# Performance work log

Hardware: AMD Instinct MI355X
Metric: run time of the kernel (lower is better)

The kernel has to match this reference:

```python
import math
import jax, jax.numpy as jnp
import numpy as np
from jax import lax

RAY_START, RAY_END = 0.5, 2.5
N_PLANES = 32

# ---- camera constants (faithful to pose_spherical / fibonacci_sphere / ImagePlanes init) ----

def _pose_spherical_np(theta, phi, radius):
    trans_t = np.array([[1,0,0,0],[0,1,0,0],[0,0,1,radius],[0,0,0,1]], dtype=np.float64)
    p = phi/180.0*np.pi
    rot_phi = np.array([[1,0,0,0],[0,np.cos(p),-np.sin(p),0],[0,np.sin(p),np.cos(p),0],[0,0,0,1]], dtype=np.float64)
    t = theta/180.0*np.pi
    rot_theta = np.array([[np.cos(t),0,-np.sin(t),0],[0,1,0,0],[np.sin(t),0,np.cos(t),0],[0,0,0,1]], dtype=np.float64)
    e = 90.0/180.0*np.pi
    rot_eta = np.array([[np.cos(e),np.sin(e),0,0],[-np.sin(e),np.cos(e),0,0],[0,0,1,0],[0,0,0,1]], dtype=np.float64)
    c2w = rot_eta @ (rot_theta @ (rot_phi @ trans_t))
    return np.array([[-1,0,0,0],[0,0,1,0],[0,1,0,0],[0,0,0,1]], dtype=np.float64) @ c2w

def _fibonacci_sphere(n):
    pts = []
    golden = math.pi*(math.sqrt(5.0)-1.0)
    for i in range(n):
        y = 1 - (i/float(n-1))*2
        r = math.sqrt(1-y*y)
        th = golden*i
        x, z = math.cos(th)*r, math.sin(th)*r
        pts.append((math.atan2(z, math.sqrt(x*x+y*y)), math.atan2(y, x)))
    return pts

_poses = np.stack([_pose_spherical_np(theta, phi, -1.307) for phi, theta in _fibonacci_sphere(N_PLANES)])
_flip = np.diag(np.array([-1.0,1.0,1.0,1.0]))
POSES34 = jnp.asarray(np.stack([np.linalg.inv(p @ _flip)[:3] for p in _poses]).astype(np.float32))  # [32,3,4]
KMAT = jnp.asarray(np.array([[1.0254,0,0.5],[0,1.0254,0.5],[0,0,1]], dtype=np.float32))  # [3,3]

# ---- grid_sample(bilinear, zeros, align_corners=False) ----

def _grid_sample(img, grid):
    # img [C,H,W], grid [P,2] (x,y) in [-1,1] -> [C,P]
    C, H, W = img.shape
    ix = ((grid[:, 0] + 1.0)*W - 1.0)*0.5
    iy = ((grid[:, 1] + 1.0)*H - 1.0)*0.5
    x0 = jnp.floor(ix); y0 = jnp.floor(iy)
    wx1 = ix - x0; wy1 = iy - y0
    def tap(xx, yy, w):
        valid = (xx >= 0) & (xx <= W - 1) & (yy >= 0) & (yy <= H - 1)
        xi = jnp.clip(xx, 0, W - 1).astype(jnp.int32)
        yi = jnp.clip(yy, 0, H - 1).astype(jnp.int32)
        return img[:, yi, xi] * (w*valid)[None, :]
    return (tap(x0, y0, (1-wx1)*(1-wy1)) + tap(x0+1, y0, wx1*(1-wy1))
            + tap(x0, y0+1, (1-wx1)*wy1) + tap(x0+1, y0+1, wx1*wy1))

# ---- ImagePlanes.forward ----

def _image_plane_feats(images, points):
    # images [32,3,H,W], points [P,3] -> [P, 96+64]
    P = points.shape[0]
    ph = jnp.concatenate([points, jnp.ones((P, 1), points.dtype)], axis=1)  # [P,4]
    cam = jnp.einsum('kij,pj->kip', POSES34, ph)            # [32,3,P]
    ps = jnp.einsum('ij,kjp->kip', KMAT, cam)                # [32,3,P]
    pix = jnp.clip(ps[:, :2, :] / ps[:, 2:3, :], 0.0, 1.0)*2.0 - 1.0  # [32,2,P]
    grid = jnp.transpose(pix, (0, 2, 1))                     # [32,P,2]
    feats = jax.vmap(_grid_sample)(images, grid)             # [32,3,P]
    feats = jnp.transpose(feats, (2, 0, 1)).reshape(P, -1)   # [P,96] plane-major
    pixflat = jnp.transpose(grid, (1, 0, 2)).reshape(P, -1)  # [P,64]
    return jnp.concatenate([feats, pixflat], axis=1)

# ---- RenderNetwork.forward (only self.net path is used) ----

def _decode(x, W1, b1, W2, b2):
    h = jax.nn.softplus(x @ W1 + b1)
    o = h @ W2 + b2
    rgb = jax.nn.sigmoid(o[..., 1:])*(1.0 + 2*0.001) - 0.001
    return rgb, o[..., 0:1]

# ---- MipRayMarcher2 ----

def _ray_march(colors, densities, depths):
    deltas = depths[:, :, 1:] - depths[:, :, :-1]
    cm = (colors[:, :, :-1] + colors[:, :, 1:])*0.5
    dm = (densities[:, :, :-1] + densities[:, :, 1:])*0.5
    zm = (depths[:, :, :-1] + depths[:, :, 1:])*0.5
    dm = jax.nn.softplus(dm - 1.0)
    alpha = 1.0 - jnp.exp(-dm*deltas)
    shifted = jnp.concatenate([jnp.ones_like(alpha[:, :, :1]), 1.0 - alpha + 1e-10], axis=2)
    weights = alpha * jnp.cumprod(shifted, axis=2)[:, :, :-1]
    rgb = jnp.sum(weights*cm, axis=2)*2.0 - 1.0
    wtot = jnp.sum(weights, axis=2)
    depth = jnp.sum(weights*zm, axis=2)/wtot
    depth = jnp.clip(jnp.where(jnp.isnan(depth), jnp.inf, depth), jnp.min(depths), jnp.max(depths))
    return rgb, depth, weights

# ---- importance sampling (sample_pdf + maxpool/avgpool smoothing) ----

def _sample_pdf(bins, weights, u, eps=1e-5):
    M = weights.shape[-1]
    weights = weights + eps
    pdf = weights / jnp.sum(weights, -1, keepdims=True)
    cdf = jnp.cumsum(pdf, -1)
    cdf = jnp.concatenate([jnp.zeros_like(cdf[:, :1]), cdf], -1)  # [R,M+1]
    inds = jax.vmap(lambda c, uu: jnp.searchsorted(c, uu, side='right'))(cdf, u)
    below = jnp.maximum(inds - 1, 0)
    above = jnp.minimum(inds, M)
    cdf_b = jnp.take_along_axis(cdf, below, 1)
    cdf_a = jnp.take_along_axis(cdf, above, 1)
    bins_b = jnp.take_along_axis(bins, below, 1)
    bins_a = jnp.take_along_axis(bins, above, 1)
    denom = jnp.where(cdf_a - cdf_b < eps, 1.0, cdf_a - cdf_b)
    return bins_b + (u - cdf_b)/denom*(bins_a - bins_b)

def _sample_importance(z_vals, weights, n_imp, u):
    B, N, S, _ = z_vals.shape
    z = z_vals.reshape(B*N, S)
    w = weights.reshape(B*N, S - 1)
    wp = jnp.pad(w, ((0, 0), (1, 1)), constant_values=-jnp.inf)
    m = jnp.maximum(wp[:, :-1], wp[:, 1:])          # max_pool1d(k=2,s=1,p=1)
    sm = (m[:, :-1] + m[:, 1:])*0.5 + 0.01           # avg_pool1d(k=2,s=1)
    samples = _sample_pdf(z, sm[:, 1:-1], u.reshape(B*N, n_imp))
    return lax.stop_gradient(samples).reshape(B, N, n_imp, 1)

# ---- full ImportanceRenderer.forward ----

def _forward(planes, ray_origins, ray_directions, strat_noise, pdf_u, W1, b1, W2, b2, D, n_imp):
    B, N = ray_origins.shape[0], ray_origins.shape[1]
    H, Wd = planes.shape[-2], planes.shape[-1]
    images = planes.reshape(B, N_PLANES, 3, H, Wd)
    delta = (RAY_END - RAY_START)/(D - 1)
    depths_c = jnp.linspace(RAY_START, RAY_END, D, dtype=planes.dtype).reshape(1, 1, D, 1) + strat_noise*delta

    def run_pass(depths):
        S = depths.shape[2]
        pts = (ray_origins[:, :, None, :] + depths*ray_directions[:, :, None, :]).reshape(B, N*S, 3)
        feats = jax.vmap(_image_plane_feats)(images, pts)  # [B,N*S,160]
        rgb, sigma = _decode(feats, W1, b1, W2, b2)
        return rgb.reshape(B, N, S, 32), sigma.reshape(B, N, S, 1)

    colors_c, dens_c = run_pass(depths_c)
    _, _, w_c = _ray_march(colors_c, dens_c, depths_c)
    depths_f = _sample_importance(depths_c, w_c, n_imp, pdf_u)
    colors_f, dens_f = run_pass(depths_f)

    all_d = jnp.concatenate([depths_c, depths_f], axis=2)
    all_c = jnp.concatenate([colors_c, colors_f], axis=2)
    all_s = jnp.concatenate([dens_c, dens_f], axis=2)
    order = jnp.argsort(all_d[..., 0], axis=2)[..., None]
    all_d = jnp.take_along_axis(all_d, order, axis=2)
    all_c = jnp.take_along_axis(all_c, order, axis=2)
    all_s = jnp.take_along_axis(all_s, order, axis=2)
    rgb_final, depth_final, w = _ray_march(all_c, all_s, all_d)
    return jnp.concatenate([rgb_final, depth_final, jnp.sum(w, axis=2)], axis=-1)  # [B,N,34]


def setup_inputs() -> dict:
    key = jax.random.key(0)
    ks = jax.random.split(key, 7)
    B, N, D, NI, H = 2, 4096, 48, 48, 64
    rd = jax.random.normal(ks[2], (B, N, 3), jnp.float32)
    rd = rd / jnp.linalg.norm(rd, axis=-1, keepdims=True)
    return {
        'planes': jax.random.normal(ks[0], (B, 96, H, H), jnp.float32),
        'ray_origins': jax.random.normal(ks[1], (B, N, 3), jnp.float32)*0.1,
        'ray_directions': rd,
        'strat_noise': jax.random.uniform(ks[3], (B, N, D, 1), jnp.float32),
        'pdf_u': jax.random.uniform(ks[4], (B, N, NI), jnp.float32),
        'W1': jax.random.normal(ks[5], (160, 64), jnp.float32)*0.05,
        'b1': jnp.zeros((64,), jnp.float32),
        'W2': jax.random.normal(ks[6], (64, 33), jnp.float32)*0.05,
        'b2': jnp.zeros((33,), jnp.float32),
        'depth_resolution': 48,
        'N_importance': 48,
    }


def reference(planes, ray_origins, ray_directions, strat_noise, pdf_u, W1, b1, W2, b2, depth_resolution, N_importance):
    return _forward(planes, ray_origins, ray_directions, strat_noise, pdf_u, W1, b1, W2, b2, depth_resolution, N_importance)
```

## Files before the change

kernel.cpp:

```cpp
#include <hip/hip_runtime.h>
#include <math.h>

#define B_   2
#define N_   4096
#define S_   48
#define NPL  32
#define NRAYS (B_*N_)
#define NPTS  (NRAYS*S_)
#define DELTA_ (2.0f/47.0f)
#define NBLK_FUSED (NPTS/256)

#define ST_XS    65
#define ST_YS    66
#define ST_PLANE (ST_YS*ST_XS)
#define SETUP_GRID 66

#define OFF_POSES  0
#define OFF_MINMAX 384
#define OFF_W1E    512
#define OFF_W2E    8704
#define OFF_B2E    10240
#define OFF_ST     16384
#define OFF_PTS    1114624
#define OFF_DC     2687488
#define OFF_DF     3080704
#define OFF_SC     3473920
#define OFF_SF     3867136
#define OFF_CC     4260352
#define OFF_CF     10551808

typedef __attribute__((ext_vector_type(8))) short short8;
typedef __attribute__((ext_vector_type(4))) float f32x4;
typedef __attribute__((ext_vector_type(2))) float f32x2;

__device__ __forceinline__ float softplus_f(float x) {
    return fmaxf(x, 0.f) + __logf(1.f + __expf(-fabsf(x)));
}
__device__ __forceinline__ float sigmoid_f(float x) {
    return __builtin_amdgcn_rcpf(1.f + __expf(-x));
}
__device__ __forceinline__ unsigned short bf16rne(float x) {
    unsigned u = __float_as_uint(x);
    u += 0x7FFFu + ((u >> 16) & 1u);
    return (unsigned short)(u >> 16);
}
__device__ __forceinline__ unsigned bf16pk(float lo, float hi) {
    return (unsigned)bf16rne(lo) | ((unsigned)bf16rne(hi) << 16);
}
__device__ __forceinline__ float bf2f(unsigned short v) {
    return __uint_as_float(((unsigned)v) << 16);
}
__device__ __forceinline__ float bflo(unsigned u) { return __uint_as_float(u << 16); }
__device__ __forceinline__ float bfhi(unsigned u) { return __uint_as_float(u & 0xffff0000u); }
__device__ __forceinline__ f32x2 unpk2(unsigned u) { return (f32x2){bflo(u), bfhi(u)}; }

__global__ __launch_bounds__(256) void k_setup(
    float* ws, const float* __restrict__ W1,
    const float* __restrict__ W2, const float* __restrict__ b2,
    const float* __restrict__ planes, const float* __restrict__ noise)
{
    __shared__ unsigned short texs[3][4096];
    __shared__ float smn[4], smx[4];
    int bid = blockIdx.x;
    int t = threadIdx.x;
    if (bid == 0) {
        unsigned short* w1e = (unsigned short*)(ws + OFF_W1E);
        for (int o = t; o < 64*256; o += 256) {
            int chunk = o >> 9, lane = (o >> 3) & 63, j = o & 7;
            int s = chunk >> 2, nt = chunk & 3, q = lane >> 4, n = lane & 15;
            int nn = nt*16 + n;
            int p = s*4 + q;
            float v = 0.f;
            if (j < 3)      v = W1[(3*p+j)*64 + nn];
            else if (j < 5) v = W1[(96 + 2*p + (j-3))*64 + nn];
            w1e[o] = bf16rne(v);
        }
        unsigned short* w2e = (unsigned short*)(ws + OFF_W2E);
        for (int o = t; o < 6*512; o += 256) {
            int chunk = o >> 9, lane = (o >> 3) & 63, j = o & 7;
            int nt = chunk >> 1, s2 = chunk & 1, q = lane >> 4, n = lane & 15;
            int nn = nt*16 + n;
            int k2 = s2*32 + q*8 + j;
            float v = (nn < 33) ? W2[k2*33 + nn] : 0.f;
            w2e[o] = bf16rne(v);
        }
        for (int idx = t; idx < 48; idx += 256)
            ws[OFF_B2E + idx] = (idx < 33) ? b2[idx] : 0.f;
    } else if (bid == 1) {
        float mn = 1e30f, mx = -1e30f;
        for (int r = t; r < NRAYS; r += 256) {
            float n0  = noise[(size_t)r*48];
            float n47 = noise[(size_t)r*48 + 47];
            mn = fminf(mn, 0.5f + n0*DELTA_);
            mx = fmaxf(mx, 0.5f + 47.f*DELTA_ + n47*DELTA_);
        }
        for (int off = 32; off > 0; off >>= 1) {
            mn = fminf(mn, __shfl_down(mn, off));
            mx = fmaxf(mx, __shfl_down(mx, off));
        }
        if ((t & 63) == 0) { smn[t >> 6] = mn; smx[t >> 6] = mx; }
        __syncthreads();
        if (t == 0) {
            ws[OFF_MINMAX]     = fminf(fminf(smn[0], smn[1]), fminf(smn[2], smn[3]));
            ws[OFF_MINMAX + 1] = fmaxf(fmaxf(smx[0], smx[1]), fmaxf(smx[2], smx[3]));
        }
    } else {
        int bp = bid - 2;
        int b = bp >> 5, p = bp & 31;
        const float* base = planes + ((size_t)b*96 + 3*p)*4096;
        for (int i = t; i < 4096; i += 256) {
            texs[0][i] = bf16rne(base[i]);
            texs[1][i] = bf16rne(base[4096 + i]);
            texs[2][i] = bf16rne(base[8192 + i]);
        }
        __syncthreads();
        uint4* qd = (uint4*)(ws + OFF_ST) + (size_t)bp*ST_PLANE;
        for (int e = t; e < ST_PLANE; e += 256) {
            int y = e / ST_XS, x = e - y*ST_XS;
            int jy = y - 1;
            unsigned a01 = 0, a2 = 0, b01 = 0, b2v = 0;
            if (jy >= 0 && jy <= 63) {
                int jxa = x - 1, jxb = x;
                if (jxa >= 0 && jxa <= 63) {
                    int ti = jy*64 + jxa;
                    a01 = (unsigned)texs[0][ti] | ((unsigned)texs[1][ti] << 16);
                    a2  = (unsigned)texs[2][ti];
                }
                if (jxb <= 63) {
                    int ti = jy*64 + jxb;
                    b01 = (unsigned)texs[0][ti] | ((unsigned)texs[1][ti] << 16);
                    b2v = (unsigned)texs[2][ti];
                }
            }
            qd[e] = make_uint4(a01, a2, b01, b2v);
        }
    }
}

__device__ __forceinline__ void proj_pt(
    const f32x2 Px, const f32x2 Py, const f32x2 Pz, const f32x2 Pw, const f32x4 Pc,
    float px, float py, float pz,
    int& eoff, float& wx, float& wy, unsigned& gpk)
{
    f32x2 c01 = Pz*pz + Pw;
    c01 = Py*py + c01;
    c01 = Px*px + c01;
    float c2 = fmaf(Pc.x,px, fmaf(Pc.y,py, fmaf(Pc.z,pz, Pc.w)));
    float rz = __builtin_amdgcn_rcpf(c2);
    f32x2 t01 = c01*1.0254f + 0.5f*c2;
    t01 = t01*rz;
    float cx = fminf(fmaxf(t01.x, 0.f), 1.f);
    float cy = fminf(fmaxf(t01.y, 0.f), 1.f);
    float gx = fmaf(2.f, cx, -1.f);
    float gy = fmaf(2.f, cy, -1.f);
    float ixp = fmaf(64.f, cx, 0.5f);
    float iyp = fmaf(64.f, cy, 0.5f);
    float xf = floorf(ixp), yf = floorf(iyp);
    wx = ixp - xf; wy = iyp - yf;
    eoff = (int)yf*ST_XS + (int)xf;
    gpk = bf16pk(gx, gy);
}

__device__ __forceinline__ void bilerp_pack(
    const uint4 r0, const uint4 r1, float wx, float wy, unsigned gpk, uint4& av)
{
    float wy0 = 1.f - wy, wy1 = wy;
    float w0x = 1.f - wx, w1x = wx;
    f32x2 tl01 = unpk2(r0.x)*wy0 + unpk2(r1.x)*wy1;
    float tl2  = fmaf(wy0, bflo(r0.y), wy1*bflo(r1.y));
    f32x2 tr01 = unpk2(r0.z)*wy0 + unpk2(r1.z)*wy1;
    float tr2  = fmaf(wy0, bflo(r0.w), wy1*bflo(r1.w));
    f32x2 f01 = tl01*w0x + tr01*w1x;
    float f2  = fmaf(w0x, tl2, w1x*tr2);
    av.x = bf16pk(f01.x, f01.y);
    av.y = ((unsigned)bf16rne(f2)) | (gpk << 16);
    av.z = gpk >> 16;
    av.w = 0u;
}

__global__ __launch_bounds__(512, 4) void k_fused(
    const uint4* __restrict__ stq, const float4* __restrict__ pts,
    const float* __restrict__ poses,
    const float* __restrict__ b1, const unsigned short* __restrict__ w1e,
    const unsigned short* __restrict__ w2e, const float* __restrict__ b2e,
    unsigned short* __restrict__ colors, float* __restrict__ dens,
    const float* __restrict__ noise, const float* __restrict__ ro,
    const float* __restrict__ rd, float* __restrict__ dcout, int coarse)
{
    __shared__ __align__(16) unsigned short w1s[16384];
    __shared__ __align__(16) unsigned short w2s[3072];
    __shared__ __align__(16) unsigned short smem[8][1152];
    __shared__ __align__(16) float pl[384];
    int tid = threadIdx.x;
    int wv = tid >> 6, lane = tid & 63;
    int n = lane & 15, q = lane >> 4;
    int bid = blockIdx.x;
    int swz = (bid & 7)*(NBLK_FUSED/8) + (bid >> 3);
    int wlocal = swz*256 + wv*32;
    int bq = (wlocal >= NPTS/2) ? 32 : 0;

    {
        const uint4* g1 = (const uint4*)w1e;
        uint4* d1 = (uint4*)w1s;
        for (int i = tid; i < 2048; i += 512) d1[i] = g1[i];
        const uint4* g2 = (const uint4*)w2e;
        uint4* d2 = (uint4*)w2s;
        if (tid < 384) { d2[tid] = g2[tid]; pl[tid] = poses[tid]; }
    }
    __syncthreads();

    float px[2], py[2], pz[2];
    if (coarse) {
#pragma unroll
        for (int t = 0; t < 2; t++) {
            int pt = wlocal + t*16 + n;
            int ray = (int)(((unsigned)(pt >> 4) * 43691u) >> 17);
            int j = pt - ray*48;
            float depth = 0.5f + (float)j*DELTA_ + noise[pt]*DELTA_;
            px[t] = fmaf(depth, rd[ray*3+0], ro[ray*3+0]);
            py[t] = fmaf(depth, rd[ray*3+1], ro[ray*3+1]);
            pz[t] = fmaf(depth, rd[ray*3+2], ro[ray*3+2]);
            if (q == 0) dcout[pt] = depth;
        }
    } else {
#pragma unroll
        for (int t = 0; t < 2; t++) {
            float4 pv = pts[wlocal + t*16 + n];
            px[t] = pv.x; py[t] = pv.y; pz[t] = pv.z;
        }
    }

    f32x4 acc[2][4];
#pragma unroll
    for (int t = 0; t < 2; t++)
#pragma unroll
        for (int nt = 0; nt < 4; nt++) {
            float bv = b1[nt*16 + n];
            acc[t][nt] = (f32x4){bv, bv, bv, bv};
        }

#pragma unroll
    for (int s = 0; s < 8; s++) {
        int plane = s*4 + q;
        const float* Pp = pl + plane*12;
        f32x2 Px = *(const f32x2*)(Pp);
        f32x2 Py = *(const f32x2*)(Pp + 2);
        f32x2 Pz = *(const f32x2*)(Pp + 4);
        f32x2 Pw = *(const f32x2*)(Pp + 6);
        f32x4 Pc = *(const f32x4*)(Pp + 8);
        const uint4* stp = stq + (unsigned)(bq + plane)*(unsigned)ST_PLANE;
        union { short8 s8; uint4 u; } av[2];
        {
            int eo0, eo1; float wx0, wy0, wx1, wy1; unsigned g0, g1;
            proj_pt(Px, Py, Pz, Pw, Pc, px[0], py[0], pz[0], eo0, wx0, wy0, g0);
            proj_pt(Px, Py, Pz, Pw, Pc, px[1], py[1], pz[1], eo1, wx1, wy1, g1);
            uint4 a0 = stp[eo0], a1 = stp[eo0 + ST_XS];
            uint4 b0 = stp[eo1], b1r = stp[eo1 + ST_XS];
            bilerp_pack(a0, a1, wx0, wy0, g0, av[0].u);
            bilerp_pack(b0, b1r, wx1, wy1, g1, av[1].u);
        }
#pragma unroll
        for (int nt = 0; nt < 4; nt++) {
            short8 bfw = *(const short8*)(w1s + ((s*4 + nt) << 9) + (lane << 3));
#pragma unroll
            for (int t = 0; t < 2; t++)
                acc[t][nt] = __builtin_amdgcn_mfma_f32_16x16x32_bf16(av[t].s8, bfw, acc[t][nt], 0, 0, 0);
        }
    }

    short8 b2f[3][2];
#pragma unroll
    for (int nt = 0; nt < 3; nt++)
#pragma unroll
        for (int s2 = 0; s2 < 2; s2++)
            b2f[nt][s2] = *(const short8*)(w2s + (((nt << 1) | s2) << 9) + (lane << 3));

    unsigned short* ht = &smem[wv][0];
#pragma unroll
    for (int t = 0; t < 2; t++) {
#pragma unroll
        for (int nt = 0; nt < 4; nt++)
#pragma unroll
            for (int r = 0; r < 4; r++) {
                float hv = softplus_f(acc[t][nt][r]);
                ht[(q*4 + r)*72 + nt*16 + n] = bf16rne(hv);
            }
        short8 a2[2];
#pragma unroll
        for (int s2 = 0; s2 < 2; s2++)
            a2[s2] = *(const short8*)(ht + n*72 + s2*32 + q*8);

        f32x4 acc2[3];
#pragma unroll
        for (int nt = 0; nt < 3; nt++) {
            float bv = b2e[nt*16 + n];
            acc2[nt] = (f32x4){bv, bv, bv, bv};
        }
#pragma unroll
        for (int nt = 0; nt < 3; nt++)
#pragma unroll
            for (int s2 = 0; s2 < 2; s2++)
                acc2[nt] = __builtin_amdgcn_mfma_f32_16x16x32_bf16(a2[s2], b2f[nt][s2], acc2[nt], 0, 0, 0);

        float* ot = (float*)ht;
#pragma unroll
        for (int nt = 0; nt < 3; nt++) {
            int col = nt*16 + n;
#pragma unroll
            for (int r = 0; r < 4; r++) {
                float v = acc2[nt][r];
                int row = q*4 + r;
                if (col == 0) ot[row*34 + 32] = v;
                else if (col <= 32) {
                    float sg = sigmoid_f(v);
                    ot[row*34 + (col-1)] = fmaf(sg, 1.002f, -0.001f);
                }
            }
        }
        unsigned* cgu = (unsigned*)(colors + (size_t)(wlocal + t*16)*32);
#pragma unroll
        for (int i = 0; i < 4; i++) {
            int ui = i*64 + lane;
            int pt = ui >> 4, ch = (ui & 15)*2;
            cgu[ui] = bf16pk(ot[pt*34 + ch], ot[pt*34 + ch + 1]);
        }
        if (lane < 16) dens[wlocal + t*16 + lane] = ot[lane*34 + 32];
    }
}

__global__ __launch_bounds__(256) void k_imp(const float* __restrict__ u, float* ws,
                                             const float* __restrict__ ro,
                                             const float* __restrict__ rd,
                                             float4* __restrict__ pts) {
    __shared__ float zl[4][48];
    __shared__ float cdfl[4][46];
    int tid = threadIdx.x;
    int wv = tid >> 6, lane = tid & 63;
    int r = blockIdx.x*4 + wv;
    const float* z   = ws + OFF_DC + (size_t)r*48;
    const float* den = ws + OFF_SC + (size_t)r*48;
    float zv = 0.f, dv = 0.f;
    if (lane < 48) { zv = z[lane]; dv = den[lane]; zl[wv][lane] = zv; }
    float zn  = __shfl_down(zv, 1);
    float dnn = __shfl_down(dv, 1);
    float alpha = 0.f, f = 1.f;
    if (lane < 47) {
        float sp = softplus_f(0.5f*(dv + dnn) - 1.f);
        alpha = 1.f - __expf(-sp*(zn - zv));
        f = 1.f - alpha + 1e-10f;
    }
    float v = f;
    for (int off = 1; off < 64; off <<= 1) { float o = __shfl_up(v, off); if (lane >= off) v *= o; }
    float T = __shfl_up(v, 1); if (lane == 0) T = 1.f;
    float w = alpha*T;
    float wn1 = __shfl_down(w, 1), wn2 = __shfl_down(w, 2);
    float pw = 0.f;
    if (lane < 45) pw = 0.5f*(fmaxf(w, wn1) + fmaxf(wn1, wn2)) + 0.01f + 1e-5f;
    float s = pw;
    for (int off = 1; off < 64; off <<= 1) { float o = __shfl_up(s, off); if (lane >= off) s += o; }
    float csum = __shfl(s, 63);
    if (lane < 45) cdfl[wv][lane+1] = s/csum;
    if (lane == 63) cdfl[wv][0] = 0.f;
    __syncthreads();
    if (lane < 48) {
        float uu = u[(size_t)r*48 + lane];
        int lo = 0, hi = 46;
        while (lo < hi) { int mid = (lo+hi)>>1; if (uu >= cdfl[wv][mid]) lo = mid+1; else hi = mid; }
        int below = max(lo-1, 0), above = min(lo, 45);
        float cb = cdfl[wv][below], ca = cdfl[wv][above];
        float zb = zl[wv][below],   za = zl[wv][above];
        float dn2 = ca - cb; if (dn2 < 1e-5f) dn2 = 1.f;
        float df_s = zb + (uu - cb)/dn2*(za - zb);
        ws[OFF_DF + (size_t)r*48 + lane] = df_s;
        float fx = fmaf(df_s, rd[r*3+0], ro[r*3+0]);
        float fy = fmaf(df_s, rd[r*3+1], ro[r*3+1]);
        float fz = fmaf(df_s, rd[r*3+2], ro[r*3+2]);
        pts[(size_t)r*48 + lane] = make_float4(fx, fy, fz, df_s);
    }
}

__global__ __launch_bounds__(256) void k_final(float* __restrict__ out, const float* __restrict__ ws,
                                               const unsigned short* __restrict__ cC,
                                               const unsigned short* __restrict__ cF)
{
    __shared__ float kd[4][96];
    __shared__ float kden[4][96];
    __shared__ float sdl[4][96];
    __shared__ float sdenl[4][96];
    __shared__ int   sidxl[4][96];
    __shared__ float warr[4][96];
    __shared__ float earr[4][96];
    int tid = threadIdx.x;
    int wv = tid >> 6, lane = tid & 63;
    int r = blockIdx.x*4 + wv;
    const float* dc = ws + OFF_DC + (size_t)r*48;
    const float* df = ws + OFF_DF + (size_t)r*48;
    const float* sc = ws + OFF_SC + (size_t)r*48;
    const float* sf = ws + OFF_SF + (size_t)r*48;
    for (int i = lane; i < 96; i += 64) {
        float d, dn;
        if (i < 48) { d = dc[i]; dn = sc[i]; }
        else        { d = df[i-48]; dn = sf[i-48]; }
        kd[wv][i] = d; kden[wv][i] = dn;
    }
    __syncthreads();
    for (int i = lane; i < 96; i += 64) {
        float d = kd[wv][i];
        int rank = 0;
        for (int j = 0; j < 96; j++) {
            float dj = kd[wv][j];
            rank += (int)((dj < d) | ((dj == d) & (j < i)));
        }
        sdl[wv][rank] = d; sdenl[wv][rank] = kden[wv][i]; sidxl[wv][rank] = i;
    }
    __syncthreads();
    int i2 = 2*lane;
    float a0=0.f, f0=1.f, a1=0.f, f1=1.f, d0=0.f, d1=0.f, d2=0.f;
    if (i2 < 95) {
        d0 = sdl[wv][i2]; d1 = sdl[wv][i2+1];
        float sp = softplus_f(0.5f*(sdenl[wv][i2] + sdenl[wv][i2+1]) - 1.f);
        a0 = 1.f - __expf(-sp*(d1 - d0)); f0 = 1.f - a0 + 1e-10f;
    }
    if (i2+1 < 95) {
        d2 = sdl[wv][i2+2];
        float sp = softplus_f(0.5f*(sdenl[wv][i2+1] + sdenl[wv][i2+2]) - 1.f);
        a1 = 1.f - __expf(-sp*(d2 - d1)); f1 = 1.f - a1 + 1e-10f;
    }
    float p = f0*f1, v = p;
    for (int off = 1; off < 64; off <<= 1) { float o = __shfl_up(v, off); if (lane >= off) v *= o; }
    float excl = __shfl_up(v, 1); if (lane == 0) excl = 1.f;
    float w0 = a0*excl, w1 = a1*excl*f0;
    if (i2   < 96) warr[wv][i2]   = w0;
    if (i2+1 < 96) warr[wv][i2+1] = w1;
    float wsm = w0 + w1;
    float dsm = w0*0.5f*(d0+d1) + w1*0.5f*(d1+d2);
    for (int off = 32; off; off >>= 1) { wsm += __shfl_xor(wsm, off); dsm += __shfl_xor(dsm, off); }
    __syncthreads();
    for (int i = lane; i < 96; i += 64) {
        float wp = (i > 0)  ? warr[wv][i-1] : 0.f;
        float wc = (i < 95) ? warr[wv][i]   : 0.f;
        earr[wv][sidxl[wv][i]] = 0.5f*(wp + wc);
    }
    __syncthreads();
    int ch = lane & 31, half = lane >> 5;
    const unsigned short* cbase = (half ? cF : cC) + ((size_t)r*48)*32 + ch;
    const float* eb = &earr[wv][half*48];
    float a = 0.f;
    for (int jj = 0; jj < 48; jj++)
        a = fmaf(eb[jj], bf2f(cbase[(size_t)jj*32]), a);
    a += __shfl_xor(a, 32);
    if (lane < 32) out[(size_t)r*34 + lane] = 2.f*a - 1.f;
    if (lane == 0) {
        float gmn = ws[OFF_MINMAX];
        float gmx = ws[OFF_MINMAX + 1];
        float depth = dsm/wsm;
        if (depth != depth) depth = __builtin_inff();
        depth = fminf(fmaxf(depth, gmn), gmx);
        out[(size_t)r*34 + 32] = depth;
        out[(size_t)r*34 + 33] = wsm;
    }
}

static void h_mul3(const double* a, const double* b, double* o) {
    for (int i = 0; i < 3; i++)
        for (int j = 0; j < 3; j++) {
            double s = 0.0;
            for (int k = 0; k < 3; k++) s += a[i*3+k]*b[k*3+j];
            o[i*3+j] = s;
        }
}

static float h_poses[384];
static bool h_poses_init = false;

static void compute_poses_host() {
    for (int t = 0; t < 32; t++) {
        double y = 1.0 - (t/31.0)*2.0;
        double rr = sqrt(fmax(1.0 - y*y, 0.0));
        double golden = M_PI*(sqrt(5.0) - 1.0);
        double th = golden*(double)t;
        double x = cos(th)*rr, z = sin(th)*rr;
        double phi   = atan2(z, sqrt(x*x + y*y));
        double theta = atan2(y, x);
        double p  = phi/180.0*M_PI;
        double tt = theta/180.0*M_PI;
        double e  = 90.0/180.0*M_PI;
        double cp = cos(p), sp = sin(p), ct = cos(tt), st = sin(tt);
        double ce = cos(e), se = sin(e);
        double Ph[9] = {1,0,0,  0,cp,-sp,  0,sp,cp};
        double Th[9] = {ct,0,-st,  0,1,0,  st,0,ct};
        double Et[9] = {ce,se,0,  -se,ce,0,  0,0,1};
        double M3[9] = {-1,0,0,  0,0,1,  0,1,0};
        double A[9], Bm[9], R[9];
        h_mul3(Th, Ph, A);
        h_mul3(Et, A, Bm);
        h_mul3(M3, Bm, R);
        double radius = -1.307;
        double tv0 = radius*R[2], tv1 = radius*R[5], tv2 = radius*R[8];
        double Rf[9] = {-R[0],R[1],R[2], -R[3],R[4],R[5], -R[6],R[7],R[8]};
        float rowv[3][4];
        for (int j = 0; j < 3; j++) {
            double r0 = Rf[0*3+j], r1 = Rf[1*3+j], r2 = Rf[2*3+j];
            rowv[j][0] = (float)r0;
            rowv[j][1] = (float)r1;
            rowv[j][2] = (float)r2;
            rowv[j][3] = (float)(-(r0*tv0 + r1*tv1 + r2*tv2));
        }
        float* P = h_poses + t*12;
        P[0] = rowv[0][0]; P[1] = rowv[1][0];
        P[2] = rowv[0][1]; P[3] = rowv[1][1];
        P[4] = rowv[0][2]; P[5] = rowv[1][2];
        P[6] = rowv[0][3]; P[7] = rowv[1][3];
        P[8] = rowv[2][0]; P[9] = rowv[2][1]; P[10] = rowv[2][2]; P[11] = rowv[2][3];
    }
}

extern "C" void kernel_launch(void* const* d_in, const int* in_sizes, int n_in,
                              void* d_out, int out_size, void* d_ws, size_t ws_size,
                              hipStream_t stream) {
    const float* planes = (const float*)d_in[0];
    const float* ro     = (const float*)d_in[1];
    const float* rd     = (const float*)d_in[2];
    const float* noise  = (const float*)d_in[3];
    const float* u      = (const float*)d_in[4];
    const float* W1     = (const float*)d_in[5];
    const float* b1     = (const float*)d_in[6];
    const float* W2     = (const float*)d_in[7];
    const float* b2     = (const float*)d_in[8];
    float* ws  = (float*)d_ws;
    float* out = (float*)d_out;
    const unsigned short* w1e = (const unsigned short*)(ws + OFF_W1E);
    const unsigned short* w2e = (const unsigned short*)(ws + OFF_W2E);
    const uint4* stq = (const uint4*)(ws + OFF_ST);
    float4* pts = (float4*)(ws + OFF_PTS);
    unsigned short* cC = (unsigned short*)(ws + OFF_CC);
    unsigned short* cF = (unsigned short*)(ws + OFF_CF);

    if (!h_poses_init) { compute_poses_host(); h_poses_init = true; }
    hipMemcpyAsync(ws + OFF_POSES, h_poses, sizeof(h_poses),
                   hipMemcpyHostToDevice, stream);

    hipLaunchKernelGGL(k_setup, dim3(SETUP_GRID), dim3(256), 0, stream,
                       ws, W1, W2, b2, planes, noise);
    hipLaunchKernelGGL(k_fused, dim3(NBLK_FUSED), dim3(512), 0, stream,
                       stq, pts, ws + OFF_POSES, b1, w1e, w2e, ws + OFF_B2E, cC, ws + OFF_SC,
                       noise, ro, rd, ws + OFF_DC, 1);
    hipLaunchKernelGGL(k_imp, dim3(NRAYS/4), dim3(256), 0, stream, u, ws, ro, rd, pts);
    hipLaunchKernelGGL(k_fused, dim3(NBLK_FUSED), dim3(512), 0, stream,
                       stq, pts, ws + OFF_POSES, b1, w1e, w2e, ws + OFF_B2E, cF, ws + OFF_SF,
                       noise, ro, rd, ws + OFF_DC, 0);
    hipLaunchKernelGGL(k_final, dim3(NRAYS/4), dim3(256), 0, stream, out, ws, cC, cF);
}
```

Baseline: 227.4 us.

## Fuse importance sampling into fine pass and compute camera poses on device

After: 224.1 us. About the same (-1.4%).

```diff
diff --git a/kernel.cpp b/kernel.cpp
--- a/kernel.cpp
+++ b/kernel.cpp
@@ -21,13 +21,12 @@
 #define OFF_W2E    8704
 #define OFF_B2E    10240
 #define OFF_ST     16384
-#define OFF_PTS    1114624
-#define OFF_DC     2687488
-#define OFF_DF     3080704
-#define OFF_SC     3473920
-#define OFF_SF     3867136
-#define OFF_CC     4260352
-#define OFF_CF     10551808
+#define OFF_DC     1114624
+#define OFF_DF     1507840
+#define OFF_SC     1901056
+#define OFF_SF     2294272
+#define OFF_CC     2687488
+#define OFF_CF     8978944
 
 typedef __attribute__((ext_vector_type(8))) short short8;
 typedef __attribute__((ext_vector_type(4))) float f32x4;
@@ -53,6 +52,18 @@
 __device__ __forceinline__ float bflo(unsigned u) { return __uint_as_float(u << 16); }
 __device__ __forceinline__ float bfhi(unsigned u) { return __uint_as_float(u & 0xffff0000u); }
 __device__ __forceinline__ f32x2 unpk2(unsigned u) { return (f32x2){bflo(u), bfhi(u)}; }
+__device__ __forceinline__ int div48(int pt) {
+    return (int)(((unsigned)(pt >> 4) * 43691u) >> 17);
+}
+
+__device__ void mul3(const double* a, const double* b, double* o) {
+    for (int i = 0; i < 3; i++)
+        for (int j = 0; j < 3; j++) {
+            double s = 0.0;
+            for (int k = 0; k < 3; k++) s += a[i*3+k]*b[k*3+j];
+            o[i*3+j] = s;
+        }
+}
 
 __global__ __launch_bounds__(256) void k_setup(
     float* ws, const float* __restrict__ W1,
@@ -64,6 +75,45 @@
     int bid = blockIdx.x;
     int t = threadIdx.x;
     if (bid == 0) {
+        if (t < 32) {
+            double y = 1.0 - (t/31.0)*2.0;
+            double rr = sqrt(fmax(1.0 - y*y, 0.0));
+            double golden = M_PI*(sqrt(5.0) - 1.0);
+            double th = golden*(double)t;
+            double x = cos(th)*rr, z = sin(th)*rr;
+            double phi   = atan2(z, sqrt(x*x + y*y));
+            double theta = atan2(y, x);
+            double p  = phi/180.0*M_PI;
+            double tt = theta/180.0*M_PI;
+            double e  = 90.0/180.0*M_PI;
+            double cp = cos(p), sp = sin(p), ct = cos(tt), st = sin(tt);
+            double ce = cos(e), se = sin(e);
+            double Ph[9] = {1,0,0,  0,cp,-sp,  0,sp,cp};
+            double Th[9] = {ct,0,-st,  0,1,0,  st,0,ct};
+            double Et[9] = {ce,se,0,  -se,ce,0,  0,0,1};
+            double M3[9] = {-1,0,0,  0,0,1,  0,1,0};
+            double A[9], Bm[9], R[9];
+            mul3(Th, Ph, A);
+            mul3(Et, A, Bm);
+            mul3(M3, Bm, R);
+            double radius = -1.307;
+            double tv0 = radius*R[2], tv1 = radius*R[5], tv2 = radius*R[8];
+            double Rf[9] = {-R[0],R[1],R[2], -R[3],R[4],R[5], -R[6],R[7],R[8]};
+            float rowv[3][4];
+            for (int j = 0; j < 3; j++) {
+                double r0 = Rf[0*3+j], r1 = Rf[1*3+j], r2 = Rf[2*3+j];
+                rowv[j][0] = (float)r0;
+                rowv[j][1] = (float)r1;
+                rowv[j][2] = (float)r2;
+                rowv[j][3] = (float)(-(r0*tv0 + r1*tv1 + r2*tv2));
+            }
+            float* P = ws + OFF_POSES + t*12;
+            P[0] = rowv[0][0]; P[1] = rowv[1][0];
+            P[2] = rowv[0][1]; P[3] = rowv[1][1];
+            P[4] = rowv[0][2]; P[5] = rowv[1][2];
+            P[6] = rowv[0][3]; P[7] = rowv[1][3];
+            P[8] = rowv[2][0]; P[9] = rowv[2][1]; P[10] = rowv[2][2]; P[11] = rowv[2][3];
+        }
         unsigned short* w1e = (unsigned short*)(ws + OFF_W1E);
         for (int o = t; o < 64*256; o += 256) {
             int chunk = o >> 9, lane = (o >> 3) & 63, j = o & 7;
@@ -179,25 +229,29 @@
 }
 
 __global__ __launch_bounds__(512, 4) void k_fused(
-    const uint4* __restrict__ stq, const float4* __restrict__ pts,
-    const float* __restrict__ poses,
+    const uint4* __restrict__ stq, const float* __restrict__ poses,
     const float* __restrict__ b1, const unsigned short* __restrict__ w1e,
     const unsigned short* __restrict__ w2e, const float* __restrict__ b2e,
     unsigned short* __restrict__ colors, float* __restrict__ dens,
     const float* __restrict__ noise, const float* __restrict__ ro,
-    const float* __restrict__ rd, float* __restrict__ dcout, int coarse)
+    const float* __restrict__ rd, const float* __restrict__ u,
+    float* __restrict__ ws, int coarse)
 {
     __shared__ __align__(16) unsigned short w1s[16384];
     __shared__ __align__(16) unsigned short w2s[3072];
     __shared__ __align__(16) unsigned short smem[8][1152];
     __shared__ __align__(16) float pl[384];
+    __shared__ float impz[6][48];
+    __shared__ float impcdf[6][46];
+    __shared__ __align__(16) float4 posl[6][48];
     int tid = threadIdx.x;
     int wv = tid >> 6, lane = tid & 63;
     int n = lane & 15, q = lane >> 4;
     int bid = blockIdx.x;
     int swz = (bid & 7)*(NBLK_FUSED/8) + (bid >> 3);
     int wlocal = swz*256 + wv*32;
-    int bq = (wlocal >= NPTS/2) ? 32 : 0;
+    int bq = (swz*256 >= NPTS/2) ? 32 : 0;
+    int r0 = (int)(((unsigned)(swz*16) * 43691u) >> 17);
 
     {
         const uint4* g1 = (const uint4*)w1e;
@@ -207,6 +261,49 @@
         uint4* d2 = (uint4*)w2s;
         if (tid < 384) { d2[tid] = g2[tid]; pl[tid] = poses[tid]; }
     }
+
+    if (!coarse && wv < 6) {
+        int r = r0 + wv;
+        const float* z   = ws + OFF_DC + (size_t)r*48;
+        const float* den = ws + OFF_SC + (size_t)r*48;
+        float zv = 0.f, dv = 0.f;
+        if (lane < 48) { zv = z[lane]; dv = den[lane]; impz[wv][lane] = zv; }
+        float zn  = __shfl_down(zv, 1);
+        float dnn = __shfl_down(dv, 1);
+        float alpha = 0.f, f = 1.f;
+        if (lane < 47) {
+            float sp = softplus_f(0.5f*(dv + dnn) - 1.f);
+            alpha = 1.f - __expf(-sp*(zn - zv));
+            f = 1.f - alpha + 1e-10f;
+        }
+        float v = f;
+        for (int off = 1; off < 64; off <<= 1) { float o = __shfl_up(v, off); if (lane >= off) v *= o; }
+        float T = __shfl_up(v, 1); if (lane == 0) T = 1.f;
+        float w = alpha*T;
+        float wn1 = __shfl_down(w, 1), wn2 = __shfl_down(w, 2);
+        float pw = 0.f;
+        if (lane < 45) pw = 0.5f*(fmaxf(w, wn1) + fmaxf(wn1, wn2)) + 0.01f + 1e-5f;
+        float s = pw;
+        for (int off = 1; off < 64; off <<= 1) { float o = __shfl_up(s, off); if (lane >= off) s += o; }
+        float csum = __shfl(s, 63);
+        if (lane < 45) impcdf[wv][lane+1] = s/csum;
+        if (lane == 63) impcdf[wv][0] = 0.f;
+        if (lane < 48) {
+            float uu = u[(size_t)r*48 + lane];
+            int lo = 0, hi = 46;
+            while (lo < hi) { int mid = (lo+hi)>>1; if (uu >= impcdf[wv][mid]) lo = mid+1; else hi = mid; }
+            int below = max(lo-1, 0), above = min(lo, 45);
+            float cb = impcdf[wv][below], ca = impcdf[wv][above];
+            float zb = impz[wv][below],   za = impz[wv][above];
+            float dn2 = ca - cb; if (dn2 < 1e-5f) dn2 = 1.f;
+            float df_s = zb + (uu - cb)/dn2*(za - zb);
+            ws[OFF_DF + (size_t)r*48 + lane] = df_s;
+            float fx = fmaf(df_s, rd[r*3+0], ro[r*3+0]);
+            float fy = fmaf(df_s, rd[r*3+1], ro[r*3+1]);
+            float fz = fmaf(df_s, rd[r*3+2], ro[r*3+2]);
+            posl[wv][lane] = make_float4(fx, fy, fz, df_s);
+        }
+    }
     __syncthreads();
 
     float px[2], py[2], pz[2];
@@ -214,18 +311,20 @@
 #pragma unroll
         for (int t = 0; t < 2; t++) {
             int pt = wlocal + t*16 + n;
-            int ray = (int)(((unsigned)(pt >> 4) * 43691u) >> 17);
+            int ray = div48(pt);
             int j = pt - ray*48;
             float depth = 0.5f + (float)j*DELTA_ + noise[pt]*DELTA_;
             px[t] = fmaf(depth, rd[ray*3+0], ro[ray*3+0]);
             py[t] = fmaf(depth, rd[ray*3+1], ro[ray*3+1]);
             pz[t] = fmaf(depth, rd[ray*3+2], ro[ray*3+2]);
-            if (q == 0) dcout[pt] = depth;
+            if (q == 0) ws[OFF_DC + pt] = depth;
         }
     } else {
 #pragma unroll
         for (int t = 0; t < 2; t++) {
-            float4 pv = pts[wlocal + t*16 + n];
+            int pt = wlocal + t*16 + n;
+            int ray = div48(pt);
+            float4 pv = posl[ray - r0][pt - ray*48];
             px[t] = pv.x; py[t] = pv.y; pz[t] = pv.z;
         }
     }
@@ -325,57 +424,6 @@
             cgu[ui] = bf16pk(ot[pt*34 + ch], ot[pt*34 + ch + 1]);
         }
         if (lane < 16) dens[wlocal + t*16 + lane] = ot[lane*34 + 32];
-    }
-}
-
-__global__ __launch_bounds__(256) void k_imp(const float* __restrict__ u, float* ws,
-                                             const float* __restrict__ ro,
-                                             const float* __restrict__ rd,
-                                             float4* __restrict__ pts) {
-    __shared__ float zl[4][48];
-    __shared__ float cdfl[4][46];
-    int tid = threadIdx.x;
-    int wv = tid >> 6, lane = tid & 63;
-    int r = blockIdx.x*4 + wv;
-    const float* z   = ws + OFF_DC + (size_t)r*48;
-    const float* den = ws + OFF_SC + (size_t)r*48;
-    float zv = 0.f, dv = 0.f;
-    if (lane < 48) { zv = z[lane]; dv = den[lane]; zl[wv][lane] = zv; }
-    float zn  = __shfl_down(zv, 1);
-    float dnn = __shfl_down(dv, 1);
-    float alpha = 0.f, f = 1.f;
-    if (lane < 47) {
-        float sp = softplus_f(0.5f*(dv + dnn) - 1.f);
-        alpha = 1.f - __expf(-sp*(zn - zv));
-        f = 1.f - alpha + 1e-10f;
-    }
-    float v = f;
-    for (int off = 1; off < 64; off <<= 1) { float o = __shfl_up(v, off); if (lane >= off) v *= o; }
-    float T = __shfl_up(v, 1); if (lane == 0) T = 1.f;
-    float w = alpha*T;
-    float wn1 = __shfl_down(w, 1), wn2 = __shfl_down(w, 2);
-    float pw = 0.f;
-    if (lane < 45) pw = 0.5f*(fmaxf(w, wn1) + fmaxf(wn1, wn2)) + 0.01f + 1e-5f;
-    float s = pw;
-    for (int off = 1; off < 64; off <<= 1) { float o = __shfl_up(s, off); if (lane >= off) s += o; }
-    float csum = __shfl(s, 63);
-    if (lane < 45) cdfl[wv][lane+1] = s/csum;
-    if (lane == 63) cdfl[wv][0] = 0.f;
-    __syncthreads();
-    if (lane < 48) {
-        float uu = u[(size_t)r*48 + lane];
-        int lo = 0, hi = 46;
-        while (lo < hi) { int mid = (lo+hi)>>1; if (uu >= cdfl[wv][mid]) lo = mid+1; else hi = mid; }
-        int below = max(lo-1, 0), above = min(lo, 45);
-        float cb = cdfl[wv][below], ca = cdfl[wv][above];
-        float zb = zl[wv][below],   za = zl[wv][above];
-        float dn2 = ca - cb; if (dn2 < 1e-5f) dn2 = 1.f;
-        float df_s = zb + (uu - cb)/dn2*(za - zb);
-        ws[OFF_DF + (size_t)r*48 + lane] = df_s;
-        float fx = fmaf(df_s, rd[r*3+0], ro[r*3+0]);
-        float fy = fmaf(df_s, rd[r*3+1], ro[r*3+1]);
-        float fz = fmaf(df_s, rd[r*3+2], ro[r*3+2]);
-        pts[(size_t)r*48 + lane] = make_float4(fx, fy, fz, df_s);
     }
 }
 
@@ -461,60 +509,6 @@
     }
 }
 
-static void h_mul3(const double* a, const double* b, double* o) {
-    for (int i = 0; i < 3; i++)
-        for (int j = 0; j < 3; j++) {
-            double s = 0.0;
-            for (int k = 0; k < 3; k++) s += a[i*3+k]*b[k*3+j];
-            o[i*3+j] = s;
-        }
-}
-
-static float h_poses[384];
-static bool h_poses_init = false;
-
-static void compute_poses_host() {
-    for (int t = 0; t < 32; t++) {
-        double y = 1.0 - (t/31.0)*2.0;
-        double rr = sqrt(fmax(1.0 - y*y, 0.0));
-        double golden = M_PI*(sqrt(5.0) - 1.0);
-        double th = golden*(double)t;
-        double x = cos(th)*rr, z = sin(th)*rr;
-        double phi   = atan2(z, sqrt(x*x + y*y));
-        double theta = atan2(y, x);
-        double p  = phi/180.0*M_PI;
-        double tt = theta/180.0*M_PI;
-        double e  = 90.0/180.0*M_PI;
-        double cp = cos(p), sp = sin(p), ct = cos(tt), st = sin(tt);
-        double ce = cos(e), se = sin(e);
-        double Ph[9] = {1,0,0,  0,cp,-sp,  0,sp,cp};
-        double Th[9] = {ct,0,-st,  0,1,0,  st,0,ct};
-        double Et[9] = {ce,se,0,  -se,ce,0,  0,0,1};
-        double M3[9] = {-1,0,0,  0,0,1,  0,1,0};
-        double A[9], Bm[9], R[9];
-        h_mul3(Th, Ph, A);
-        h_mul3(Et, A, Bm);
-        h_mul3(M3, Bm, R);
-        double radius = -1.307;
-        double tv0 = radius*R[2], tv1 = radius*R[5], tv2 = radius*R[8];
-        double Rf[9] = {-R[0],R[1],R[2], -R[3],R[4],R[5], -R[6],R[7],R[8]};
-        float rowv[3][4];
-        for (int j = 0; j < 3; j++) {
-            double r0 = Rf[0*3+j], r1 = Rf[1*3+j], r2 = Rf[2*3+j];
-            rowv[j][0] = (float)r0;
-            rowv[j][1] = (float)r1;
-            rowv[j][2] = (float)r2;
-            rowv[j][3] = (float)(-(r0*tv0 + r1*tv1 + r2*tv2));
-        }
-        float* P = h_poses + t*12;
-        P[0] = rowv[0][0]; P[1] = rowv[1][0];
-        P[2] = rowv[0][1]; P[3] = rowv[1][1];
-        P[4] = rowv[0][2]; P[5] = rowv[1][2];
-        P[6] = rowv[0][3]; P[7] = rowv[1][3];
-        P[8] = rowv[2][0]; P[9] = rowv[2][1]; P[10] = rowv[2][2]; P[11] = rowv[2][3];
-    }
-}
-
 extern "C" void kernel_launch(void* const* d_in, const int* in_sizes, int n_in,
                               void* d_out, int out_size, void* d_ws, size_t ws_size,
                               hipStream_t stream) {
@@ -532,22 +526,16 @@
     const unsigned short* w1e = (const unsigned short*)(ws + OFF_W1E);
     const unsigned short* w2e = (const unsigned short*)(ws + OFF_W2E);
     const uint4* stq = (const uint4*)(ws + OFF_ST);
-    float4* pts = (float4*)(ws + OFF_PTS);
     unsigned short* cC = (unsigned short*)(ws + OFF_CC);
     unsigned short* cF = (unsigned short*)(ws + OFF_CF);
-
-    if (!h_poses_init) { compute_poses_host(); h_poses_init = true; }
-    hipMemcpyAsync(ws + OFF_POSES, h_poses, sizeof(h_poses),
-                   hipMemcpyHostToDevice, stream);
 
     hipLaunchKernelGGL(k_setup, dim3(SETUP_GRID), dim3(256), 0, stream,
                        ws, W1, W2, b2, planes, noise);
     hipLaunchKernelGGL(k_fused, dim3(NBLK_FUSED), dim3(512), 0, stream,
-                       stq, pts, ws + OFF_POSES, b1, w1e, w2e, ws + OFF_B2E, cC, ws + OFF_SC,
-                       noise, ro, rd, ws + OFF_DC, 1);
-    hipLaunchKernelGGL(k_imp, dim3(NRAYS/4), dim3(256), 0, stream, u, ws, ro, rd, pts);
+                       stq, ws + OFF_POSES, b1, w1e, w2e, ws + OFF_B2E, cC, ws + OFF_SC,
+                       noise, ro, rd, u, ws, 1);
     hipLaunchKernelGGL(k_fused, dim3(NBLK_FUSED), dim3(512), 0, stream,
-                       stq, pts, ws + OFF_POSES, b1, w1e, w2e, ws + OFF_B2E, cF, ws + OFF_SF,
-                       noise, ro, rd, ws + OFF_DC, 0);
+                       stq, ws + OFF_POSES, b1, w1e, w2e, ws + OFF_B2E, cF, ws + OFF_SF,
+                       noise, ro, rd, u, ws, 0);
     hipLaunchKernelGGL(k_final, dim3(NRAYS/4), dim3(256), 0, stream, out, ws, cC, cF);
 }
```
